# Kernel optimization log

Hardware: AMD Instinct MI355X
Metric: run time of the kernel (lower is better)

## Reference

```python
import jax, jax.numpy as jnp
import numpy as np

L_SEG = 20   # number of CFT segments (hard-coded in original forward)
M_CHEB = 8   # Chebyshev quadrature order per segment


def _cft_magnitude(x, modes):
    """|CFT(x)| at integer frequencies [0, modes).

    Faithful to vectorized_batched_cft_decomposed with L=20, M=8, but only
    evaluated at the first `modes` frequencies (identical values; the original
    computes all rfft freqs then slices). Segment loop is folded into a single
    einsum by absorbing the per-segment phase shift into the quadrature weights.
    x: (B, C, N) real. Returns (B, C, modes) float.
    """
    n = x.shape[-1]
    t = jnp.linspace(0.0, 1.0, n)
    freqs = jnp.arange(modes, dtype=x.dtype)  # rfftfreq(n, d=1/n)[:modes]
    seg_len = 1.0 / L_SEG
    starts = jnp.linspace(0.0, 1.0, L_SEG + 1)[:-1]  # (L,)
    k = jnp.arange(M_CHEB, dtype=x.dtype)
    cheb = -jnp.cos((2.0 * k + 1.0) * jnp.pi / (2.0 * M_CHEB))  # (M,) nodes in [-1,1]
    T = jnp.cos(k[:, None] * jnp.arccos(cheb)[None, :])  # (K=M, M) Chebyshev T_k at nodes
    angle = cheb[:, None] * (freqs[None, :] * (2.0 * jnp.pi * seg_len / 2.0))  # (M, F)
    Wr = jnp.einsum('km,mf->kf', T, jnp.cos(angle)) * (seg_len / 2.0)  # (M, F)
    Wi = jnp.einsum('km,mf->kf', T, -jnp.sin(angle)) * (seg_len / 2.0)
    # piecewise-linear interpolation of x at the Chebyshev nodes of every segment
    t_seg = starts[:, None] + seg_len / 2.0 * (cheb + 1.0)[None, :]  # (L, M)
    right = jnp.clip(jnp.searchsorted(t, t_seg), 0, n - 1)
    left = jnp.clip(right - 1, 0, None)
    t_l, t_r = t[left], t[right]
    denom = jnp.where(t_r - t_l == 0.0, 1.0, t_r - t_l)
    w_r = (t_seg - t_l) / denom
    w_l = 1.0 - w_r
    seg = w_l * x[:, :, left] + w_r * x[:, :, right]  # (B, C, L, M)
    # per-segment phase shift exp(-i*2*pi*f*a) folded into combined weights
    phi = 2.0 * jnp.pi * starts[:, None] * freqs[None, :]  # (L, F)
    cs, sn = jnp.cos(phi), jnp.sin(phi)
    Ar = Wr[None] * cs[:, None, :] + Wi[None] * sn[:, None, :]   # (L, M, F)
    Ai = -Wr[None] * sn[:, None, :] + Wi[None] * cs[:, None, :]
    real = jnp.einsum('bclm,lmf->bcf', seg, Ar)
    imag = jnp.einsum('bclm,lmf->bcf', seg, Ai)
    return jnp.sqrt(real * real + imag * imag)


def setup_inputs() -> dict:
    key = jax.random.key(0)
    ks = jax.random.split(key, 4)
    B, Cin, Cout, N, modes = 32, 64, 64, 8192, 32
    scale = 1.0 / (Cin * Cout)
    return {
        'x': jax.random.normal(ks[0], (B, Cin, N), dtype=jnp.float32),
        'w1_real': scale * jax.random.uniform(ks[1], (Cin, Cout, modes), dtype=jnp.float32),
        'w1_imag': scale * jax.random.uniform(ks[2], (Cin, Cout, modes), dtype=jnp.float32),
        'gate_w': jax.random.normal(ks[3], (Cout, Cin), dtype=jnp.float32) / np.sqrt(Cin),
        'ln_gamma': jnp.ones((modes,), dtype=jnp.float32),
        'ln_beta': jnp.zeros((modes,), dtype=jnp.float32),
    }


def reference(x, w1_real, w1_imag, gate_w, ln_gamma, ln_beta):
    n = x.shape[-1]
    n_rfft = n // 2 + 1
    modes = w1_real.shape[-1]
    x_fft = jnp.fft.rfft(x)  # (B, C, n_rfft) complex64
    # CFT magnitude is detached in the original (x_cft.detach())
    mag = jax.lax.stop_gradient(_cft_magnitude(x, modes))  # (B, C, modes)
    # LayerNorm over the modes axis (eps = 1e-5, torch default)
    mu = jnp.mean(mag, axis=-1, keepdims=True)
    var = jnp.mean((mag - mu) ** 2, axis=-1, keepdims=True)
    g_norm = (mag - mu) / jnp.sqrt(var + 1e-5) * ln_gamma + ln_beta
    # 1x1 conv (no bias) over channels, then sigmoid gate
    gate = jax.nn.sigmoid(jnp.einsum('oi,bif->bof', gate_w, g_norm))  # (B, Cout, modes)
    gated = x_fft[:, :, :modes] * gate  # requires Cin == Cout
    w1 = w1_real + 1j * w1_imag  # (Cin, Cout, modes) complex
    out_modes = jnp.einsum('bix,iox->box', gated, w1)
    pad = jnp.zeros(out_modes.shape[:2] + (n_rfft - modes,), dtype=out_modes.dtype)
    out_ft = jnp.concatenate([out_modes, pad], axis=-1)
    return jnp.fft.irfft(out_ft, n=n)
```

## Files before the change

kernel.cpp:

```cpp
#include <hip/hip_runtime.h>
#include <hip/hip_bf16.h>
#include <math.h>

#define NN    8192
#define NROWS 2048
#define FF    32
#define LM    160

static constexpr int TRIG  = 0;
static constexpr int W1RT  = 524288;
static constexpr int W1IT  = 655360;
static constexpr int GWT   = 786432;
static constexpr int AR_   = 790528;
static constexpr int AI_   = 795648;
static constexpr int WL_   = 800768;
static constexpr int WR_   = 800928;
static constexpr int IL_   = 801088;
static constexpr int IR_   = 801248;
static constexpr int XR_   = 801408;
static constexpr int XI_   = 866944;
static constexpr int GN_   = 932480;
static constexpr int ARAI  = 998016;

#define PI_D 3.14159265358979323846

__global__ __launch_bounds__(256) void k_trig(float* __restrict__ ws) {
  int idx = blockIdx.x * 256 + threadIdx.x;
  int k4 = idx >> 8, f = (idx >> 2) & 63, j = idx & 3;
  int n = 4 * k4 + j;
  int fr = f & 31;
  int p = (fr * n) & (NN - 1);
  float ang = (float)p * (float)(2.0 * PI_D / (double)NN);
  float s, c;
  sincosf(ang, &s, &c);
  ws[TRIG + idx] = (f < 32) ? c : s;
}

__global__ __launch_bounds__(256) void k_cft_tables(float* __restrict__ ws) {
  int tid = blockIdx.x * 256 + threadIdx.x;
  if (tid >= LM * FF) return;
  int j = tid >> 5, f = tid & 31;
  int l = j >> 3, m = j & 7;
  double cheb[8];
  #pragma unroll
  for (int mm = 0; mm < 8; ++mm)
    cheb[mm] = -cos((2.0 * mm + 1.0) * PI_D / 16.0);

  double Wr = 0.0, Wi = 0.0;
  #pragma unroll
  for (int mm = 0; mm < 8; ++mm) {
    double T = cos((double)m * acos(cheb[mm]));
    double ang = cheb[mm] * (double)f * (PI_D * 0.05);
    Wr += T * cos(ang);
    Wi += T * (-sin(ang));
  }
  Wr *= 0.025; Wi *= 0.025;
  double phi = 2.0 * PI_D * ((double)l * 0.05) * (double)f;
  double cs = cos(phi), sn = sin(phi);
  ws[AR_ + j * FF + f] = (float)(Wr * cs + Wi * sn);
  ws[AI_ + j * FF + f] = (float)(-Wr * sn + Wi * cs);

  if (f == 0) {
    double v = (double)l * 0.05 + 0.025 * (cheb[m] + 1.0);
    int r = (int)(v * 8191.0);
    while ((double)r / 8191.0 < v) ++r;
    while (r > 0 && (double)(r - 1) / 8191.0 >= v) --r;
    if (r > 8191) r = 8191;
    int le = r - 1; if (le < 0) le = 0;
    double tl = (double)le / 8191.0, tr = (double)r / 8191.0;
    double den = (tr - tl == 0.0) ? 1.0 : (tr - tl);
    double wr = (v - tl) / den;
    ws[WL_ + j] = (float)(1.0 - wr);
    ws[WR_ + j] = (float)wr;
    ((int*)ws)[IL_ + j] = le;
    ((int*)ws)[IR_ + j] = r;
  }
}

__global__ __launch_bounds__(256) void k_transpose(const float* __restrict__ w1r,
                                                   const float* __restrict__ w1i,
                                                   const float* __restrict__ gw,
                                                   float* __restrict__ ws) {
  int idx = blockIdx.x * 256 + threadIdx.x;
  if (idx >= 32 * 64 * 64) return;
  int o = idx & 63, i = (idx >> 6) & 63, f = idx >> 12;
  ws[W1RT + (f * 64 + i) * 64 + o] = w1r[(i * 64 + o) * FF + f];
  ws[W1IT + (f * 64 + i) * 64 + o] = w1i[(i * 64 + o) * FF + f];
  if (idx < 4096) {
    ws[GWT + idx] = gw[(idx & 63) * 64 + (idx >> 6)];
  }
}

__global__ __launch_bounds__(256, 4) void k_fwd_gemm(const float* __restrict__ x,
                                                     const float* __restrict__ ws,
                                                     float* __restrict__ part) {
  __shared__ __align__(16) float xs[64 * 128];
  const int rt = blockIdx.x >> 5, kc = blockIdx.x & 31;
  const int t = threadIdx.x;
  const int w = t >> 6, lane = t & 63;
  const int rblock = rt * 64;
  const float4* __restrict__ tg4 = (const float4*)(ws + TRIG);

  float acc[16];
  #pragma unroll
  for (int r = 0; r < 16; ++r) acc[r] = 0.f;

  const int c4 = t & 31, r0 = t >> 5;
  for (int st = 0; st < 2; ++st) {
    const int kb = kc * 256 + st * 128;
    __syncthreads();
    #pragma unroll
    for (int p = 0; p < 8; ++p) {
      int row = r0 + 8 * p;
      float4 v = *(const float4*)(x + (size_t)(rblock + row) * NN + kb + c4 * 4);
      *(float4*)(&xs[row * 128 + c4 * 4]) = v;
    }
    __syncthreads();
    const int k40 = (kb >> 2);
    for (int it = 0; it < 32; ++it) {
      float4 tg = tg4[(size_t)(k40 + it) * 64 + lane];
      const float* xw = &xs[(w * 16) * 128 + it * 4];
      #pragma unroll
      for (int r = 0; r < 16; ++r) {
        float4 xv = *(const float4*)(xw + r * 128);
        acc[r] = fmaf(xv.w, tg.w, fmaf(xv.z, tg.z, fmaf(xv.y, tg.y, fmaf(xv.x, tg.x, acc[r]))));
      }
    }
  }
  float* __restrict__ pp = part + ((size_t)kc * NROWS + rblock + w * 16) * 64 + lane;
  #pragma unroll
  for (int r = 0; r < 16; ++r)
    pp[(size_t)r * 64] = acc[r];
}

__global__ __launch_bounds__(256) void k_fred(const float* __restrict__ part,
                                              float* __restrict__ ws) {
  int idx = blockIdx.x * 256 + threadIdx.x;
  int row = idx >> 6, f = idx & 63;
  float s = 0.f;
  #pragma unroll
  for (int kc = 0; kc < 32; ++kc)
    s += part[((size_t)kc * NROWS + row) * 64 + f];
  if (f < 32) ws[XR_ + row * FF + f] = s;
  else        ws[XI_ + row * FF + (f - 32)] = -s;
}

__global__ __launch_bounds__(256) void k_cft(const float* __restrict__ x,
                                             const float* __restrict__ gamma,
                                             const float* __restrict__ beta,
                                             float* __restrict__ ws) {
  const int sub = threadIdx.x >> 6, li = threadIdx.x & 63;
  const int row = blockIdx.x * 4 + sub;
  const float* __restrict__ xr = x + (size_t)row * NN;
  __shared__ float seg[4][LM];
  #pragma unroll
  for (int g = 0; g < 3; ++g) {
    int j = li + 64 * g;
    if (j < LM) {
      int il = ((const int*)ws)[IL_ + j];
      int ir = ((const int*)ws)[IR_ + j];
      seg[sub][j] = ws[WL_ + j] * xr[il] + ws[WR_ + j] * xr[ir];
    }
  }
  __syncthreads();
  if (li < FF) {
    float re = 0.f, im = 0.f;
    #pragma unroll 8
    for (int j = 0; j < LM; ++j) {
      float sv = seg[sub][j];
      re = fmaf(sv, ws[AR_ + j * FF + li], re);
      im = fmaf(sv, ws[AI_ + j * FF + li], im);
    }
    float mag = sqrtf(re * re + im * im);
    float mu = mag;
    mu += __shfl_xor(mu, 1);  mu += __shfl_xor(mu, 2);  mu += __shfl_xor(mu, 4);
    mu += __shfl_xor(mu, 8);  mu += __shfl_xor(mu, 16);
    mu *= (1.0f / 32.0f);
    float d = mag - mu;
    float vv = d * d;
    vv += __shfl_xor(vv, 1);  vv += __shfl_xor(vv, 2);  vv += __shfl_xor(vv, 4);
    vv += __shfl_xor(vv, 8);  vv += __shfl_xor(vv, 16);
    vv *= (1.0f / 32.0f);
    float g = d / sqrtf(vv + 1e-5f) * gamma[li] + beta[li];
    ws[GN_ + row * FF + li] = g;
  }
}

__global__ __launch_bounds__(64) void k_gate(float* __restrict__ ws) {
  int bidx = blockIdx.x;
  int b = bidx >> 5, f = bidx & 31;
  int o = threadIdx.x;
  __shared__ float gn[64], gr[64], gi[64];
  int rowb = b * 64;
  gn[o] = ws[GN_ + (rowb + o) * FF + f];
  float xre = ws[XR_ + (rowb + o) * FF + f];
  float xim = ws[XI_ + (rowb + o) * FF + f];
  __syncthreads();
  float acc = 0.f;
  #pragma unroll 16
  for (int i = 0; i < 64; ++i)
    acc = fmaf(ws[GWT + i * 64 + o], gn[i], acc);
  float gate = 1.0f / (1.0f + expf(-acc));
  gr[o] = xre * gate;
  gi[o] = xim * gate;
  __syncthreads();
  float Yr = 0.f, Yi = 0.f;
  const float* __restrict__ w1rt = ws + W1RT + f * 4096;
  const float* __restrict__ w1it = ws + W1IT + f * 4096;
  #pragma unroll 8
  for (int i = 0; i < 64; ++i) {
    float a = gr[i], bb2 = gi[i];
    float wr = w1rt[i * 64 + o], wi = w1it[i * 64 + o];
    Yr = fmaf(a, wr, Yr); Yr = fmaf(-bb2, wi, Yr);
    Yi = fmaf(a, wi, Yi); Yi = fmaf(bb2, wr, Yi);
  }
  float* A = ws + ARAI + (size_t)(rowb + o) * 64;
  if (f == 0) {
    A[0]  = Yr * (1.0f / (float)NN);
    A[32] = 0.0f;
  } else {
    A[f]      = Yr * (2.0f / (float)NN);
    A[32 + f] = -Yi * (2.0f / (float)NN);
  }
}

__global__ __launch_bounds__(256) void k_inv(const float* __restrict__ ws,
                                             float* __restrict__ out) {
  __shared__ __align__(16) float T_s[64 * 256];
  int blk = blockIdx.x;
  int bb = blk >> 5, cc = blk & 31;
  int t = threadIdx.x;
  int cx = t & 15, ry = t >> 4;

  {
    const int base4 = cc * 64;
    #pragma unroll
    for (int r2 = 0; r2 < 16; ++r2) {
      int q = t + 256 * r2;
      int f = q & 63, c4 = q >> 6;
      float4 v = *(const float4*)(ws + TRIG + (size_t)((base4 + c4) * 64 + f) * 4);
      *(float4*)(&T_s[f * 256 + c4 * 4]) = v;
    }
  }
  __syncthreads();

  float acc[4][16];
  #pragma unroll
  for (int r = 0; r < 4; ++r)
    #pragma unroll
    for (int k = 0; k < 16; ++k) acc[r][k] = 0.f;

  const float* __restrict__ Ab = ws + ARAI + (size_t)(bb * 64) * 64;
  for (int j0 = 0; j0 < 64; j0 += 4) {
    float4 av[4];
    #pragma unroll
    for (int r = 0; r < 4; ++r)
      av[r] = *(const float4*)(Ab + (ry * 4 + r) * 64 + j0);
    #pragma unroll
    for (int jj = 0; jj < 4; ++jj) {
      int j = j0 + jj;
      const float* Trow = &T_s[j * 256 + cx * 4];
      float4 t0 = *(const float4*)(Trow);
      float4 t1 = *(const float4*)(Trow + 64);
      float4 t2 = *(const float4*)(Trow + 128);
      float4 t3 = *(const float4*)(Trow + 192);
      #pragma unroll
      for (int r = 0; r < 4; ++r) {
        float a = ((const float*)&av[r])[jj];
        acc[r][0]  = fmaf(a, t0.x, acc[r][0]);
        acc[r][1]  = fmaf(a, t0.y, acc[r][1]);
        acc[r][2]  = fmaf(a, t0.z, acc[r][2]);
        acc[r][3]  = fmaf(a, t0.w, acc[r][3]);
        acc[r][4]  = fmaf(a, t1.x, acc[r][4]);
        acc[r][5]  = fmaf(a, t1.y, acc[r][5]);
        acc[r][6]  = fmaf(a, t1.z, acc[r][6]);
        acc[r][7]  = fmaf(a, t1.w, acc[r][7]);
        acc[r][8]  = fmaf(a, t2.x, acc[r][8]);
        acc[r][9]  = fmaf(a, t2.y, acc[r][9]);
        acc[r][10] = fmaf(a, t2.z, acc[r][10]);
        acc[r][11] = fmaf(a, t2.w, acc[r][11]);
        acc[r][12] = fmaf(a, t3.x, acc[r][12]);
        acc[r][13] = fmaf(a, t3.y, acc[r][13]);
        acc[r][14] = fmaf(a, t3.z, acc[r][14]);
        acc[r][15] = fmaf(a, t3.w, acc[r][15]);
      }
    }
  }
  #pragma unroll
  for (int r = 0; r < 4; ++r) {
    int row = bb * 64 + ry * 4 + r;
    float* op = out + (size_t)row * NN + cc * 256;
    #pragma unroll
    for (int q = 0; q < 4; ++q) {
      float4 v = make_float4(acc[r][4*q+0], acc[r][4*q+1], acc[r][4*q+2], acc[r][4*q+3]);
      *(float4*)(op + q * 64 + cx * 4) = v;
    }
  }
}

extern "C" void kernel_launch(void* const* d_in, const int* in_sizes, int n_in,
                              void* d_out, int out_size, void* d_ws, size_t ws_size,
                              hipStream_t stream) {
  const float* x     = (const float*)d_in[0];
  const float* w1r   = (const float*)d_in[1];
  const float* w1i   = (const float*)d_in[2];
  const float* gw    = (const float*)d_in[3];
  const float* gamma = (const float*)d_in[4];
  const float* beta  = (const float*)d_in[5];
  float* out = (float*)d_out;
  float* ws = (float*)d_ws;
  float* part = (float*)d_out;

  hipLaunchKernelGGL(k_trig,       dim3(2048), dim3(256), 0, stream, ws);
  hipLaunchKernelGGL(k_cft_tables, dim3(20),   dim3(256), 0, stream, ws);
  hipLaunchKernelGGL(k_transpose,  dim3(512),  dim3(256), 0, stream, w1r, w1i, gw, ws);
  hipLaunchKernelGGL(k_fwd_gemm,   dim3(1024), dim3(256), 0, stream, x, ws, part);
  hipLaunchKernelGGL(k_fred,       dim3(512),  dim3(256), 0, stream, part, ws);
  hipLaunchKernelGGL(k_cft,        dim3(512),  dim3(256), 0, stream, x, gamma, beta, ws);
  hipLaunchKernelGGL(k_gate,       dim3(1024), dim3(64),  0, stream, ws);
  hipLaunchKernelGGL(k_inv,        dim3(1024), dim3(256), 0, stream, ws, out);
}
```

Measured before the change: 213.9 us.

## Split forward DFT GEMM finer and rework inverse GEMM with transposed trig table

```diff
diff --git a/kernel.cpp b/kernel.cpp
--- a/kernel.cpp
+++ b/kernel.cpp
@@ -7,20 +7,21 @@
 #define FF    32
 #define LM    160
 
-static constexpr int TRIG  = 0;
-static constexpr int W1RT  = 524288;
-static constexpr int W1IT  = 655360;
-static constexpr int GWT   = 786432;
-static constexpr int AR_   = 790528;
-static constexpr int AI_   = 795648;
-static constexpr int WL_   = 800768;
-static constexpr int WR_   = 800928;
-static constexpr int IL_   = 801088;
-static constexpr int IR_   = 801248;
-static constexpr int XR_   = 801408;
-static constexpr int XI_   = 866944;
-static constexpr int GN_   = 932480;
-static constexpr int ARAI  = 998016;
+static constexpr int TRIG   = 0;
+static constexpr int W1RT   = 524288;
+static constexpr int W1IT   = 655360;
+static constexpr int GWT    = 786432;
+static constexpr int AR_    = 790528;
+static constexpr int AI_    = 795648;
+static constexpr int WL_    = 800768;
+static constexpr int WR_    = 800928;
+static constexpr int IL_    = 801088;
+static constexpr int IR_    = 801248;
+static constexpr int XR_    = 801408;
+static constexpr int XI_    = 866944;
+static constexpr int GN_    = 932480;
+static constexpr int ARAI   = 998016;
+static constexpr int TRIGT_ = 1129088;
 
 #define PI_D 3.14159265358979323846
 
@@ -33,7 +34,9 @@
   float ang = (float)p * (float)(2.0 * PI_D / (double)NN);
   float s, c;
   sincosf(ang, &s, &c);
-  ws[TRIG + idx] = (f < 32) ? c : s;
+  float v = (f < 32) ? c : s;
+  ws[TRIG + idx] = v;
+  ws[TRIGT_ + f * NN + n] = v;
 }
 
 __global__ __launch_bounds__(256) void k_cft_tables(float* __restrict__ ws) {
@@ -91,42 +94,54 @@
   }
 }
 
-__global__ __launch_bounds__(256, 4) void k_fwd_gemm(const float* __restrict__ x,
-                                                     const float* __restrict__ ws,
-                                                     float* __restrict__ part) {
+__global__ __launch_bounds__(256) void k_fwd_gemm(const float* __restrict__ x,
+                                                  const float* __restrict__ ws,
+                                                  float* __restrict__ part) {
   __shared__ __align__(16) float xs[64 * 128];
-  const int rt = blockIdx.x >> 5, kc = blockIdx.x & 31;
+  const int rt = blockIdx.x >> 6, kc = blockIdx.x & 63;
   const int t = threadIdx.x;
   const int w = t >> 6, lane = t & 63;
   const int rblock = rt * 64;
   const float4* __restrict__ tg4 = (const float4*)(ws + TRIG);
+  const int k40 = kc * 32;
+
+  float4 tg = tg4[(size_t)k40 * 64 + lane];
+
+  const int c4 = t & 31, r0 = t >> 5;
+  const int kb = kc * 128;
+  #pragma unroll
+  for (int p = 0; p < 8; ++p) {
+    int row = r0 + 8 * p;
+    float4 v = *(const float4*)(x + (size_t)(rblock + row) * NN + kb + c4 * 4);
+    *(float4*)(&xs[row * 128 + c4 * 4]) = v;
+  }
 
   float acc[16];
   #pragma unroll
   for (int r = 0; r < 16; ++r) acc[r] = 0.f;
 
-  const int c4 = t & 31, r0 = t >> 5;
-  for (int st = 0; st < 2; ++st) {
-    const int kb = kc * 256 + st * 128;
-    __syncthreads();
-    #pragma unroll
-    for (int p = 0; p < 8; ++p) {
-      int row = r0 + 8 * p;
-      float4 v = *(const float4*)(x + (size_t)(rblock + row) * NN + kb + c4 * 4);
-      *(float4*)(&xs[row * 128 + c4 * 4]) = v;
-    }
-    __syncthreads();
-    const int k40 = (kb >> 2);
-    for (int it = 0; it < 32; ++it) {
-      float4 tg = tg4[(size_t)(k40 + it) * 64 + lane];
-      const float* xw = &xs[(w * 16) * 128 + it * 4];
-      #pragma unroll
-      for (int r = 0; r < 16; ++r) {
-        float4 xv = *(const float4*)(xw + r * 128);
-        acc[r] = fmaf(xv.w, tg.w, fmaf(xv.z, tg.z, fmaf(xv.y, tg.y, fmaf(xv.x, tg.x, acc[r]))));
-      }
-    }
-  }
+  __syncthreads();
+
+#define FWD_STEP(IT, TGV)                                                       \
+  {                                                                             \
+    const float* xw = &xs[(w * 16) * 128 + (IT) * 4];                           \
+    _Pragma("unroll")                                                           \
+    for (int r = 0; r < 16; ++r) {                                              \
+      float4 xv = *(const float4*)(xw + r * 128);                               \
+      acc[r] = fmaf(xv.w, (TGV).w, fmaf(xv.z, (TGV).z,                          \
+               fmaf(xv.y, (TGV).y, fmaf(xv.x, (TGV).x, acc[r]))));              \
+    }                                                                           \
+  }
+
+  #pragma unroll 4
+  for (int it = 0; it < 31; ++it) {
+    float4 tgn = tg4[(size_t)(k40 + it + 1) * 64 + lane];
+    FWD_STEP(it, tg);
+    tg = tgn;
+  }
+  FWD_STEP(31, tg);
+#undef FWD_STEP
+
   float* __restrict__ pp = part + ((size_t)kc * NROWS + rblock + w * 16) * 64 + lane;
   #pragma unroll
   for (int r = 0; r < 16; ++r)
@@ -138,8 +153,8 @@
   int idx = blockIdx.x * 256 + threadIdx.x;
   int row = idx >> 6, f = idx & 63;
   float s = 0.f;
-  #pragma unroll
-  for (int kc = 0; kc < 32; ++kc)
+  #pragma unroll 8
+  for (int kc = 0; kc < 64; ++kc)
     s += part[((size_t)kc * NROWS + row) * 64 + f];
   if (f < 32) ws[XR_ + row * FF + f] = s;
   else        ws[XI_ + row * FF + (f - 32)] = -s;
@@ -226,75 +241,66 @@
 
 __global__ __launch_bounds__(256) void k_inv(const float* __restrict__ ws,
                                              float* __restrict__ out) {
-  __shared__ __align__(16) float T_s[64 * 256];
-  int blk = blockIdx.x;
-  int bb = blk >> 5, cc = blk & 31;
-  int t = threadIdx.x;
-  int cx = t & 15, ry = t >> 4;
-
-  {
-    const int base4 = cc * 64;
-    #pragma unroll
-    for (int r2 = 0; r2 < 16; ++r2) {
-      int q = t + 256 * r2;
-      int f = q & 63, c4 = q >> 6;
-      float4 v = *(const float4*)(ws + TRIG + (size_t)((base4 + c4) * 64 + f) * 4);
-      *(float4*)(&T_s[f * 256 + c4 * 4]) = v;
-    }
-  }
-  __syncthreads();
-
-  float acc[4][16];
-  #pragma unroll
-  for (int r = 0; r < 4; ++r)
-    #pragma unroll
-    for (int k = 0; k < 16; ++k) acc[r][k] = 0.f;
-
-  const float* __restrict__ Ab = ws + ARAI + (size_t)(bb * 64) * 64;
-  for (int j0 = 0; j0 < 64; j0 += 4) {
-    float4 av[4];
-    #pragma unroll
-    for (int r = 0; r < 4; ++r)
-      av[r] = *(const float4*)(Ab + (ry * 4 + r) * 64 + j0);
-    #pragma unroll
-    for (int jj = 0; jj < 4; ++jj) {
-      int j = j0 + jj;
-      const float* Trow = &T_s[j * 256 + cx * 4];
-      float4 t0 = *(const float4*)(Trow);
-      float4 t1 = *(const float4*)(Trow + 64);
-      float4 t2 = *(const float4*)(Trow + 128);
-      float4 t3 = *(const float4*)(Trow + 192);
-      #pragma unroll
-      for (int r = 0; r < 4; ++r) {
-        float a = ((const float*)&av[r])[jj];
-        acc[r][0]  = fmaf(a, t0.x, acc[r][0]);
-        acc[r][1]  = fmaf(a, t0.y, acc[r][1]);
-        acc[r][2]  = fmaf(a, t0.z, acc[r][2]);
-        acc[r][3]  = fmaf(a, t0.w, acc[r][3]);
-        acc[r][4]  = fmaf(a, t1.x, acc[r][4]);
-        acc[r][5]  = fmaf(a, t1.y, acc[r][5]);
-        acc[r][6]  = fmaf(a, t1.z, acc[r][6]);
-        acc[r][7]  = fmaf(a, t1.w, acc[r][7]);
-        acc[r][8]  = fmaf(a, t2.x, acc[r][8]);
-        acc[r][9]  = fmaf(a, t2.y, acc[r][9]);
-        acc[r][10] = fmaf(a, t2.z, acc[r][10]);
-        acc[r][11] = fmaf(a, t2.w, acc[r][11]);
-        acc[r][12] = fmaf(a, t3.x, acc[r][12]);
-        acc[r][13] = fmaf(a, t3.y, acc[r][13]);
-        acc[r][14] = fmaf(a, t3.z, acc[r][14]);
-        acc[r][15] = fmaf(a, t3.w, acc[r][15]);
-      }
-    }
-  }
-  #pragma unroll
-  for (int r = 0; r < 4; ++r) {
-    int row = bb * 64 + ry * 4 + r;
-    float* op = out + (size_t)row * NN + cc * 256;
-    #pragma unroll
-    for (int q = 0; q < 4; ++q) {
-      float4 v = make_float4(acc[r][4*q+0], acc[r][4*q+1], acc[r][4*q+2], acc[r][4*q+3]);
-      *(float4*)(op + q * 64 + cx * 4) = v;
-    }
+  __shared__ __align__(16) float As[32 * 64];
+  const int blk = blockIdx.x;
+  const int bb = blk >> 5, cc = blk & 31;
+  const int t = threadIdx.x;
+  const int w = t >> 6, lane = t & 63;
+  const int rowbase = bb * 32;
+  const float* __restrict__ trigt = ws + TRIGT_;
+  const int colb = cc * 256 + lane * 4;
+
+  float4 tg0 = *(const float4*)(trigt + (size_t)0 * NN + colb);
+  float4 tg1 = *(const float4*)(trigt + (size_t)1 * NN + colb);
+  float4 tg2 = *(const float4*)(trigt + (size_t)2 * NN + colb);
+  float4 tg3 = *(const float4*)(trigt + (size_t)3 * NN + colb);
+
+  #pragma unroll
+  for (int p = 0; p < 2; ++p) {
+    int idx = t + 256 * p;
+    int r = idx >> 4, q = idx & 15;
+    *(float4*)(&As[r * 64 + q * 4]) =
+        *(const float4*)(ws + ARAI + (size_t)(rowbase + r) * 64 + q * 4);
+  }
+
+  float4 acc[8];
+  #pragma unroll
+  for (int r = 0; r < 8; ++r) acc[r] = make_float4(0.f, 0.f, 0.f, 0.f);
+
+  __syncthreads();
+
+#define INV_STEP(F0)                                                            \
+  {                                                                             \
+    _Pragma("unroll")                                                           \
+    for (int r = 0; r < 8; ++r) {                                               \
+      float4 av = *(const float4*)(&As[(w * 8 + r) * 64 + (F0)]);               \
+      acc[r].x = fmaf(av.x, tg0.x, acc[r].x); acc[r].y = fmaf(av.x, tg0.y, acc[r].y); \
+      acc[r].z = fmaf(av.x, tg0.z, acc[r].z); acc[r].w = fmaf(av.x, tg0.w, acc[r].w); \
+      acc[r].x = fmaf(av.y, tg1.x, acc[r].x); acc[r].y = fmaf(av.y, tg1.y, acc[r].y); \
+      acc[r].z = fmaf(av.y, tg1.z, acc[r].z); acc[r].w = fmaf(av.y, tg1.w, acc[r].w); \
+      acc[r].x = fmaf(av.z, tg2.x, acc[r].x); acc[r].y = fmaf(av.z, tg2.y, acc[r].y); \
+      acc[r].z = fmaf(av.z, tg2.z, acc[r].z); acc[r].w = fmaf(av.z, tg2.w, acc[r].w); \
+      acc[r].x = fmaf(av.w, tg3.x, acc[r].x); acc[r].y = fmaf(av.w, tg3.y, acc[r].y); \
+      acc[r].z = fmaf(av.w, tg3.z, acc[r].z); acc[r].w = fmaf(av.w, tg3.w, acc[r].w); \
+    }                                                                           \
+  }
+
+  for (int fo = 0; fo < 15; ++fo) {
+    int f0 = fo * 4;
+    float4 n0 = *(const float4*)(trigt + (size_t)(f0 + 4) * NN + colb);
+    float4 n1 = *(const float4*)(trigt + (size_t)(f0 + 5) * NN + colb);
+    float4 n2 = *(const float4*)(trigt + (size_t)(f0 + 6) * NN + colb);
+    float4 n3 = *(const float4*)(trigt + (size_t)(f0 + 7) * NN + colb);
+    INV_STEP(f0);
+    tg0 = n0; tg1 = n1; tg2 = n2; tg3 = n3;
+  }
+  INV_STEP(60);
+#undef INV_STEP
+
+  #pragma unroll
+  for (int r = 0; r < 8; ++r) {
+    int row = rowbase + w * 8 + r;
+    *(float4*)(out + (size_t)row * NN + colb) = acc[r];
   }
 }
 
@@ -314,9 +320,9 @@
   hipLaunchKernelGGL(k_trig,       dim3(2048), dim3(256), 0, stream, ws);
   hipLaunchKernelGGL(k_cft_tables, dim3(20),   dim3(256), 0, stream, ws);
   hipLaunchKernelGGL(k_transpose,  dim3(512),  dim3(256), 0, stream, w1r, w1i, gw, ws);
-  hipLaunchKernelGGL(k_fwd_gemm,   dim3(1024), dim3(256), 0, stream, x, ws, part);
+  hipLaunchKernelGGL(k_fwd_gemm,   dim3(2048), dim3(256), 0, stream, x, ws, part);
   hipLaunchKernelGGL(k_fred,       dim3(512),  dim3(256), 0, stream, part, ws);
   hipLaunchKernelGGL(k_cft,        dim3(512),  dim3(256), 0, stream, x, gamma, beta, ws);
   hipLaunchKernelGGL(k_gate,       dim3(1024), dim3(64),  0, stream, ws);
-  hipLaunchKernelGGL(k_inv,        dim3(1024), dim3(256), 0, stream, ws, out);
-}
+  hipLaunchKernelGGL(k_inv,        dim3(2048), dim3(256), 0, stream, ws, out);
+}
```

Measured after the change: 216.7 us. No clear change (+1.3%).
